# Optimization experiments

Measured on AMD Instinct MI355X. Metric: run time of the kernel, lower is better.

## Reference

```python
import jax, jax.numpy as jnp
import numpy as np

PAD = 32       # F.pad(..., (32,32,32,32))
N_INST = 32    # labels in [0, 32]; one-hot drops background -> 32 instance channels
EPS = 1e-6


def _lovasz_hinge_flat(logits, labels):
    # logits, labels: [P] flattened over instances*H*W (per_image=False)
    signs = 2.0 * labels - 1.0
    errors = 1.0 - logits * signs
    order = jnp.argsort(-errors)               # descending sort of errors
    errors_sorted = errors[order]
    labels_sorted = labels[order]
    gts = jnp.sum(labels_sorted)
    inter = gts - jnp.cumsum(labels_sorted)
    union = gts + jnp.cumsum(1.0 - labels_sorted)
    jaccard = 1.0 - inter / union
    grad = jnp.concatenate([jaccard[:1], jaccard[1:] - jaccard[:-1]])
    return jnp.dot(jax.nn.relu(errors_sorted), jax.lax.stop_gradient(grad))


def _per_image_loss(emb, w, gt, W1, b1, W2, b2):
    # emb: [C,H,W], w: [1,H,W], gt: [1,H,W] int
    emb = jnp.pad(emb, ((0, 0), (PAD, PAD), (PAD, PAD)))
    w = jnp.pad(w, ((0, 0), (PAD, PAD), (PAD, PAD)))[0]      # [H',W']
    gt = jnp.pad(gt, ((0, 0), (PAD, PAD), (PAD, PAD)))[0]    # [H',W']
    # one-hot over instance ids 1..N_INST (background dropped): [N,H',W']
    oh = (gt[None, :, :] == jnp.arange(1, N_INST + 1)[:, None, None]).astype(emb.dtype)
    # weighted per-instance counts and centroids
    counts = jnp.einsum('nhw,hw->n', oh, w) + EPS                     # [N]
    centers = jnp.einsum('nhw,chw,hw->nc', oh, emb, w) / counts[:, None]  # [N,C]
    # sims = centers broadcast minus embeddings: [N,C,H',W']
    sims = centers[:, :, None, None] - emb[None]
    # per-pixel classifier MLP (flatten -> Linear -> ReLU -> Linear -> fold)
    h = jax.nn.relu(jnp.einsum('nchw,ck->nkhw', sims, W1) + b1[None, :, None, None])
    logits = jnp.einsum('nkhw,k->nhw', h, W2[:, 0]) + b2[0]           # probs[:,0]
    return _lovasz_hinge_flat(logits.reshape(-1), oh.reshape(-1))


def setup_inputs() -> dict:
    key = jax.random.key(0)
    k = jax.random.split(key, 8)
    B, C, H, Wd, HID = 4, 16, 192, 192, 32
    return {
        'y_embeddings': jax.random.normal(k[0], (B, C, H, Wd), jnp.float32),
        'y_weights': jax.random.uniform(k[1], (B, 1, H, Wd), jnp.float32),
        'y_true': jax.random.randint(k[2], (B, 1, H, Wd), 0, N_INST + 1),
        'W1': jax.random.normal(k[3], (C, HID), jnp.float32) * 0.1,
        'b1': jnp.zeros((HID,), jnp.float32),
        'W2': jax.random.normal(k[4], (HID, 1), jnp.float32) * 0.1,
        'b2': jnp.zeros((1,), jnp.float32),
    }


def reference(y_embeddings, y_weights, y_true, W1, b1, W2, b2):
    # random labels over 192^2 pixels guarantee every image has positives,
    # so the torch `if torch.any(gt>0)` branch is always taken -> plain mean.
    losses = jax.vmap(_per_image_loss, in_axes=(0, 0, 0, None, None, None, None))(
        y_embeddings, y_weights, y_true, W1, b1, W2, b2)
    return jnp.mean(losses)
```

## Files before the change

kernel.cpp:

```cpp
#include <hip/hip_runtime.h>

#define NBINS 2048
#define B 4
#define C 16
#define HID 32
#define NI 32
#define INTER 36864
#define PADMULT 28672
#define EPSF 1e-6f
#define THR 256
#define BPI 144
#define NBLK (B * BPI)
#define INIT_BLK 64

#define OFF_COUNTS 0
#define OFF_CSUMS  (OFF_COUNTS + B*NI)
#define OFF_V      (OFF_CSUMS + B*NI*C)
#define OFF_PERR   (OFF_V + B*NI*HID)
#define OFF_MKEY   (OFF_PERR + B*NI)
#define OFF_RANGE  (OFF_MKEY + B)
#define OFF_DONE0  (OFF_RANGE + 2*B)
#define OFF_DONE1  (OFF_DONE0 + B)
#define CTRL_END   (OFF_DONE1 + B)
#define OFF_F64    8192

__device__ inline unsigned fmap(float f) {
    unsigned u = __float_as_uint(f);
    return (u & 0x80000000u) ? ~u : (u | 0x80000000u);
}
__device__ inline float funmap(unsigned k) {
    return (k & 0x80000000u) ? __uint_as_float(k & 0x7fffffffu)
                             : __uint_as_float(~k);
}
__device__ inline float aload_f(const float* p) {
    return __hip_atomic_load(p, __ATOMIC_RELAXED, __HIP_MEMORY_SCOPE_AGENT);
}
__device__ inline unsigned aload_u(const unsigned* p) {
    return __hip_atomic_load(p, __ATOMIC_RELAXED, __HIP_MEMORY_SCOPE_AGENT);
}
__device__ inline unsigned long long aload_u64(const unsigned long long* p) {
    return __hip_atomic_load(p, __ATOMIC_RELAXED, __HIP_MEMORY_SCOPE_AGENT);
}
__device__ inline void release_atomics() {
    asm volatile("s_waitcnt vmcnt(0)" ::: "memory");
}

__global__ void k_init(unsigned* wsu, float* out) {
    unsigned gtid = blockIdx.x * 256u + threadIdx.x;
    for (unsigned i = gtid; i < CTRL_END; i += INIT_BLK * 256u) wsu[i] = 0u;
    unsigned* f = wsu + OFF_F64;
    for (unsigned i = gtid; i < B * NBINS * 2; i += INIT_BLK * 256u) f[i] = 0u;
    if (gtid == 0) out[0] = 0.f;
}

__global__ __launch_bounds__(THR, 4) void k_stats(
        const float* __restrict__ emb, const float* __restrict__ wgt,
        const int* __restrict__ gt, const float* __restrict__ W1,
        const float* __restrict__ b1, const float* __restrict__ W2,
        const float* __restrict__ b2, float* ws, unsigned* wsu) {
    struct SSt { float cnt[NI]; float sum[NI * 17]; };
    struct SCt { float v[NI * HID]; float a[HID]; float stage[NI * (C + 1)]; };
    __shared__ union { SSt st; SCt ct; } sm;
    __shared__ unsigned s_mk, s_lo, s_hi;
    __shared__ int s_last;
    int tid = threadIdx.x, bx = blockIdx.x;
    int img = bx / BPI;
    int q = (bx - img * BPI) * THR + tid;
    for (int i = tid; i < NI; i += THR) sm.st.cnt[i] = 0.f;
    for (int i = tid; i < NI * 17; i += THR) sm.st.sum[i] = 0.f;
    if (tid == 0) s_mk = 0u;
    __syncthreads();

    int g = gt[img * INTER + q];
    const float* ep = emb + (size_t)img * C * INTER + q;
    float e[C];
    float nrm = 0.f;
    #pragma unroll
    for (int c = 0; c < C; c++) { e[c] = ep[c * INTER]; nrm = fmaf(e[c], e[c], nrm); }
    if (g > 0) {
        float wv = wgt[img * INTER + q];
        atomicAdd(&sm.st.cnt[g - 1], wv);
        #pragma unroll
        for (int c = 0; c < C; c++)
            atomicAdd(&sm.st.sum[(g - 1) * 17 + c], e[c] * wv);
    }
    atomicMax(&s_mk, fmap(nrm));
    __syncthreads();
    for (int i = tid; i < NI; i += THR)
        atomicAdd(&ws[OFF_COUNTS + img * NI + i], sm.st.cnt[i]);
    for (int i = tid; i < NI * C; i += THR) {
        int n = i / C, c = i - n * C;
        atomicAdd(&ws[OFF_CSUMS + (img * NI + n) * C + c], sm.st.sum[n * 17 + c]);
    }
    if (tid == 0) atomicMax(&wsu[OFF_MKEY + img], s_mk);

    release_atomics();
    __syncthreads();
    if (tid == 0)
        s_last = (atomicAdd(&wsu[OFF_DONE0 + img], 1u) == (unsigned)(BPI - 1));
    __syncthreads();
    if (!s_last) return;

    int im = img;
    for (int i = tid; i < NI * (C + 1); i += THR) {
        float v = (i < NI) ? aload_f(&ws[OFF_COUNTS + im * NI + i])
                           : aload_f(&ws[OFF_CSUMS + im * NI * C + (i - NI)]);
        sm.ct.stage[i] = v;
    }
    float b2v = b2[0];
    float M = sqrtf(funmap(aload_u(&wsu[OFF_MKEY + im])));
    if (tid < HID) {
        float ssq = 0.f;
        #pragma unroll
        for (int c = 0; c < C; c++)
            ssq = fmaf(W1[c * HID + tid], W1[c * HID + tid], ssq);
        sm.ct.a[tid] = M * sqrtf(ssq);
    }
    if (tid == 0) { s_lo = 0xFFFFFFFFu; s_hi = 0u; }
    __syncthreads();
    for (int idx = tid; idx < NI * HID; idx += THR) {
        int n = idx >> 5, k = idx & 31;
        float cv = sm.ct.stage[n] + EPSF;
        float acc = b1[k];
        #pragma unroll
        for (int c = 0; c < C; c++)
            acc += (sm.ct.stage[NI + n * C + c] / cv) * W1[c * HID + k];
        sm.ct.v[idx] = acc;
        ws[OFF_V + im * NI * HID + idx] = acc;
    }
    __syncthreads();
    if (tid < NI) {
        float lo = b2v, hi = b2v, lgp = b2v;
        #pragma unroll
        for (int k = 0; k < HID; k++) {
            float vk = sm.ct.v[tid * HID + k], a = sm.ct.a[k], w = W2[k];
            float thi = fmaxf(vk + a, 0.f), tlo = fmaxf(vk - a, 0.f);
            hi += w * (w > 0.f ? thi : tlo);
            lo += w * (w > 0.f ? tlo : thi);
            lgp = fmaf(fmaxf(vk, 0.f), w, lgp);
        }
        float pe = 1.f + lgp;
        ws[OFF_PERR + im * NI + tid] = pe;
        atomicMin(&s_lo, fmap(fminf(1.f - hi, 1.f + lo)));
        atomicMax(&s_hi, fmap(fmaxf(1.f - lo, 1.f + hi)));
    }
    __syncthreads();
    if (tid == 0) {
        ((float*)wsu)[OFF_RANGE + im * 2]     = funmap(s_lo);
        ((float*)wsu)[OFF_RANGE + im * 2 + 1] = funmap(s_hi);
    }
}

struct SMemLoss { unsigned cnt[NBINS]; unsigned pos[NBINS]; float sum[NBINS];
                  unsigned pc[THR]; unsigned pp[THR]; double a[THR]; };

__global__ __launch_bounds__(THR, 4) void k_hist(
        const float* __restrict__ emb, const int* __restrict__ gt,
        const float* __restrict__ W1, const float* __restrict__ W2,
        const float* __restrict__ b2, const float* __restrict__ ws,
        unsigned* wsu, float* out) {
    __shared__ union { unsigned h[NBINS]; SMemLoss ls; } sm;
    __shared__ int s_last;
    int tid = threadIdx.x, bx = blockIdx.x;
    int img = bx / BPI;
    int q = (bx - img * BPI) * THR + tid;
    for (int i = tid; i < NBINS; i += THR) sm.h[i] = 0u;
    float emin = ((const float*)wsu)[OFF_RANGE + img * 2];
    float emax = ((const float*)wsu)[OFF_RANGE + img * 2 + 1];
    float invbw = (float)NBINS / fmaxf(emax - emin, 1e-20f);
    float b2v = b2[0];
    const float* vimg = ws + OFF_V + img * NI * HID;
    __syncthreads();

    const float* ep = emb + (size_t)img * C * INTER + q;
    float u[HID];
    #pragma unroll
    for (int k = 0; k < HID; k++) u[k] = 0.f;
    #pragma unroll
    for (int c = 0; c < C; c++) {
        float ev = ep[c * INTER];
        #pragma unroll
        for (int k = 0; k < HID; k++) u[k] = fmaf(ev, W1[c * HID + k], u[k]);
    }
    int g = gt[img * INTER + q];
    #pragma unroll 4
    for (int n = 0; n < NI; n++) {
        const float* vn = vimg + n * HID;
        float lg0 = b2v, lg1 = 0.f, lg2 = 0.f, lg3 = 0.f;
        #pragma unroll
        for (int k = 0; k < HID; k += 4) {
            lg0 = fmaf(fmaxf(vn[k + 0] - u[k + 0], 0.f), W2[k + 0], lg0);
            lg1 = fmaf(fmaxf(vn[k + 1] - u[k + 1], 0.f), W2[k + 1], lg1);
            lg2 = fmaf(fmaxf(vn[k + 2] - u[k + 2], 0.f), W2[k + 2], lg2);
            lg3 = fmaf(fmaxf(vn[k + 3] - u[k + 3], 0.f), W2[k + 3], lg3);
        }
        float lg = (lg0 + lg1) + (lg2 + lg3);
        bool pos = (g == n + 1);
        float err = pos ? (1.f - lg) : (1.f + lg);
        int bn = (int)((emax - err) * invbw);
        bn = bn < 0 ? 0 : (bn >= NBINS ? NBINS - 1 : bn);
        atomicAdd(&sm.h[bn], pos ? 0x10001u : 1u);
    }
    __syncthreads();
    unsigned long long* f64 = (unsigned long long*)(wsu + OFF_F64) + (size_t)img * NBINS;
    for (int i = tid; i < NBINS; i += THR) {
        unsigned pk = sm.h[i];
        if (pk)
            atomicAdd(&f64[i], (unsigned long long)(pk & 0xFFFFu)
                             | ((unsigned long long)(pk >> 16) << 32));
    }

    release_atomics();
    __syncthreads();
    if (tid == 0)
        s_last = (atomicAdd(&wsu[OFF_DONE1 + img], 1u) == (unsigned)(BPI - 1));
    __syncthreads();
    if (!s_last) return;

    {
        const int T = THR, CHUNK = NBINS / THR;
        int im = img;
        float bw = (emax - emin) / (float)NBINS;
        for (int i = tid; i < NBINS; i += T) {
            unsigned long long pk = aload_u64(&f64[i]);
            unsigned cv = (unsigned)(pk & 0xFFFFFFFFu);
            sm.ls.cnt[i] = cv;
            sm.ls.pos[i] = (unsigned)(pk >> 32);
            float center = emax - ((float)i + 0.5f) * bw;
            sm.ls.sum[i] = (float)cv * fmaxf(center, 0.f);
        }
        __syncthreads();
        if (tid < NI) {
            float pe = ws[OFF_PERR + im * NI + tid];
            int bn = (int)((emax - pe) * invbw);
            bn = bn < 0 ? 0 : (bn >= NBINS ? NBINS - 1 : bn);
            atomicAdd(&sm.ls.cnt[bn], (unsigned)PADMULT);
            atomicAdd(&sm.ls.sum[bn], (float)PADMULT * fmaxf(pe, 0.f));
        }
        __syncthreads();
        unsigned ccnt = 0, cpos = 0;
        for (int j = 0; j < CHUNK; j++) {
            int bn = tid * CHUNK + j;
            ccnt += sm.ls.cnt[bn]; cpos += sm.ls.pos[bn];
        }
        sm.ls.pc[tid] = ccnt; sm.ls.pp[tid] = cpos;
        __syncthreads();
        for (int off = 1; off < T; off <<= 1) {
            unsigned ac = 0, ap = 0;
            if (tid >= off) { ac = sm.ls.pc[tid - off]; ap = sm.ls.pp[tid - off]; }
            __syncthreads();
            sm.ls.pc[tid] += ac; sm.ls.pp[tid] += ap;
            __syncthreads();
        }
        double Gd = (double)sm.ls.pp[T - 1];
        double r = (double)(sm.ls.pc[tid] - ccnt);
        double L = (double)(sm.ls.pp[tid] - cpos);
        double Jprev = 1.0 - (Gd - L) / (Gd + r - L);
        double acc = 0.0;
        for (int j = 0; j < CHUNK; j++) {
            int bn = tid * CHUNK + j;
            unsigned cv = sm.ls.cnt[bn], pv = sm.ls.pos[bn];
            if (cv) {
                r += (double)cv; L += (double)pv;
                double J = 1.0 - (Gd - L) / (Gd + r - L);
                double mean = (double)sm.ls.sum[bn] / (double)cv;
                acc += mean * (J - Jprev);
                Jprev = J;
            }
        }
        sm.ls.a[tid] = acc;
        __syncthreads();
        for (int s = T / 2; s > 0; s >>= 1) {
            if (tid < s) sm.ls.a[tid] += sm.ls.a[tid + s];
            __syncthreads();
        }
        if (tid == 0) atomicAdd(out, (float)(sm.ls.a[0] * 0.25));
    }
}

extern "C" void kernel_launch(void* const* d_in, const int* in_sizes, int n_in,
                              void* d_out, int out_size, void* d_ws, size_t ws_size,
                              hipStream_t stream) {
    const float* emb = (const float*)d_in[0];
    const float* wgt = (const float*)d_in[1];
    const int*   gt  = (const int*)d_in[2];
    const float* W1  = (const float*)d_in[3];
    const float* b1  = (const float*)d_in[4];
    const float* W2  = (const float*)d_in[5];
    const float* b2  = (const float*)d_in[6];
    float* out = (float*)d_out;
    float* ws  = (float*)d_ws;
    unsigned* wsu = (unsigned*)d_ws;

    k_init<<<INIT_BLK, 256, 0, stream>>>(wsu, out);
    k_stats<<<NBLK, THR, 0, stream>>>(emb, wgt, gt, W1, b1, W2, b2, ws, wsu);
    k_hist<<<NBLK, THR, 0, stream>>>(emb, gt, W1, W2, b2, ws, wsu, out);
}
```

Measured before the change: 137.7 us.

## Split hist kernel instance loop across two blocks and move histogram zeroing into stats

k_hist now launches twice as many blocks, and each block handles half of the 32 instances for its pixel tile. This raises parallelism from 576 to 1152 blocks, at the cost of recomputing the per-pixel hidden projection u in both halves. Zeroing of the 64-bit global histogram moves from k_init into k_stats, so k_init shrinks to a single block clearing only the control words. The risks are duplicated embedding loads, duplicated W1 work, and more global histogram atomics.

```diff
diff --git a/kernel.cpp b/kernel.cpp
--- a/kernel.cpp
+++ b/kernel.cpp
@@ -11,7 +11,10 @@
 #define THR 256
 #define BPI 144
 #define NBLK (B * BPI)
-#define INIT_BLK 64
+#define NSPL 2
+#define NIH (NI / NSPL)
+#define BPIH (BPI * NSPL)
+#define NBLKH (B * BPIH)
 
 #define OFF_COUNTS 0
 #define OFF_CSUMS  (OFF_COUNTS + B*NI)
@@ -46,11 +49,10 @@
 }
 
 __global__ void k_init(unsigned* wsu, float* out) {
-    unsigned gtid = blockIdx.x * 256u + threadIdx.x;
-    for (unsigned i = gtid; i < CTRL_END; i += INIT_BLK * 256u) wsu[i] = 0u;
-    unsigned* f = wsu + OFF_F64;
-    for (unsigned i = gtid; i < B * NBINS * 2; i += INIT_BLK * 256u) f[i] = 0u;
-    if (gtid == 0) out[0] = 0.f;
+    int tid = threadIdx.x;
+    for (int i = tid; i < OFF_V; i += 256) wsu[i] = 0u;
+    for (int i = OFF_MKEY + tid; i < CTRL_END; i += 256) wsu[i] = 0u;
+    if (tid == 0) out[0] = 0.f;
 }
 
 __global__ __launch_bounds__(THR, 4) void k_stats(
@@ -66,6 +68,11 @@
     int tid = threadIdx.x, bx = blockIdx.x;
     int img = bx / BPI;
     int q = (bx - img * BPI) * THR + tid;
+    {
+        unsigned gtid = (unsigned)bx * THR + tid;
+        if (gtid < B * NBINS)
+            ((unsigned long long*)(wsu + OFF_F64))[gtid] = 0ull;
+    }
     for (int i = tid; i < NI; i += THR) sm.st.cnt[i] = 0.f;
     for (int i = tid; i < NI * 17; i += THR) sm.st.sum[i] = 0.f;
     if (tid == 0) s_mk = 0u;
@@ -162,8 +169,11 @@
     __shared__ union { unsigned h[NBINS]; SMemLoss ls; } sm;
     __shared__ int s_last;
     int tid = threadIdx.x, bx = blockIdx.x;
-    int img = bx / BPI;
-    int q = (bx - img * BPI) * THR + tid;
+    int img = bx / BPIH;
+    int sub = bx - img * BPIH;
+    int tile = sub >> 1, half = sub & 1;
+    int q = tile * THR + tid;
+    int n0 = half * NIH;
     for (int i = tid; i < NBINS; i += THR) sm.h[i] = 0u;
     float emin = ((const float*)wsu)[OFF_RANGE + img * 2];
     float emax = ((const float*)wsu)[OFF_RANGE + img * 2 + 1];
@@ -184,7 +194,8 @@
     }
     int g = gt[img * INTER + q];
     #pragma unroll 4
-    for (int n = 0; n < NI; n++) {
+    for (int nn = 0; nn < NIH; nn++) {
+        int n = n0 + nn;
         const float* vn = vimg + n * HID;
         float lg0 = b2v, lg1 = 0.f, lg2 = 0.f, lg3 = 0.f;
         #pragma unroll
@@ -213,7 +224,7 @@
     release_atomics();
     __syncthreads();
     if (tid == 0)
-        s_last = (atomicAdd(&wsu[OFF_DONE1 + img], 1u) == (unsigned)(BPI - 1));
+        s_last = (atomicAdd(&wsu[OFF_DONE1 + img], 1u) == (unsigned)(BPIH - 1));
     __syncthreads();
     if (!s_last) return;
 
@@ -292,7 +303,7 @@
     float* ws  = (float*)d_ws;
     unsigned* wsu = (unsigned*)d_ws;
 
-    k_init<<<INIT_BLK, 256, 0, stream>>>(wsu, out);
+    k_init<<<1, 256, 0, stream>>>(wsu, out);
     k_stats<<<NBLK, THR, 0, stream>>>(emb, wgt, gt, W1, b1, W2, b2, ws, wsu);
-    k_hist<<<NBLK, THR, 0, stream>>>(emb, gt, W1, W2, b2, ws, wsu, out);
-}
+    k_hist<<<NBLKH, THR, 0, stream>>>(emb, gt, W1, W2, b2, ws, wsu, out);
+}
```

Result: no change. 139.4 us (+1.2%).
